# Kernel optimization log

Measured on AMD Instinct MI355X. Metric: run time of the kernel, lower is better.

The kernel has to match this reference:

```python
import jax, jax.numpy as jnp
import numpy as np

EPS = 1e-5


def gcn_conv(x, W, b, src, dst, ew, num_nodes):
    """GCNConv with add_self_loops=True, symmetric normalization (PyG default)."""
    # degree at destination, self-loop weight 1.0 included implicitly
    deg = jax.ops.segment_sum(ew, dst, num_segments=num_nodes) + 1.0  # [N]
    dinv = jax.lax.rsqrt(deg)                                         # deg >= 1
    norm = dinv[src] * ew * dinv[dst]                                 # [E]
    h = x @ W                                                         # [N, F]
    msg = norm[:, None] * h[src]                                      # [E, F]
    agg = jax.ops.segment_sum(msg, dst, num_segments=num_nodes)       # [N, F]
    # self-loop contribution: dinv[i] * 1 * dinv[i] = 1/deg[i]
    agg = agg + h * (1.0 / deg)[:, None]
    return agg + b


def batchnorm(h, gamma, beta):
    mean = jnp.mean(h, axis=0)
    var = jnp.mean(jnp.square(h - mean), axis=0)  # biased, training-mode stats
    return (h - mean) * jax.lax.rsqrt(var + EPS) * gamma + beta


def setup_inputs() -> dict:
    key = jax.random.key(0)
    ks = jax.random.split(key, 8)
    N, E, F = 50000, 800000, 64
    x = jax.random.normal(ks[0], (N, F), dtype=jnp.float32)
    edge_index = jax.random.randint(ks[1], (2, E), 0, N, dtype=jnp.int64)
    edge_weight = jax.random.uniform(ks[2], (E,), dtype=jnp.float32)
    s = 1.0 / np.sqrt(F)
    W1 = jax.random.uniform(ks[3], (F, F), jnp.float32, -s, s)
    b1 = jnp.zeros((F,), jnp.float32)
    W2 = jax.random.uniform(ks[4], (F, F), jnp.float32, -s, s)
    b2 = jnp.zeros((F,), jnp.float32)
    gamma1 = jnp.ones((F,), jnp.float32)
    beta1 = jnp.zeros((F,), jnp.float32)
    gamma2 = jnp.ones((F,), jnp.float32)
    beta2 = jnp.zeros((F,), jnp.float32)
    return {"x": x, "edge_index": edge_index, "edge_weight": edge_weight,
            "W1": W1, "b1": b1, "gamma1": gamma1, "beta1": beta1,
            "W2": W2, "b2": b2, "gamma2": gamma2, "beta2": beta2}


def reference(x, edge_index, edge_weight, W1, b1, gamma1, beta1, W2, b2, gamma2, beta2):
    N = x.shape[0]
    src, dst = edge_index[0], edge_index[1]
    identity = x
    out = gcn_conv(x, W1, b1, src, dst, edge_weight, N)
    out = jax.nn.relu(batchnorm(out, gamma1, beta1))
    out = gcn_conv(out, W2, b2, src, dst, edge_weight, N)
    out = batchnorm(out, gamma2, beta2)
    out = out + identity  # residual: num_input_features == hidden_dim
    return jax.nn.relu(out)
```

## Files before the change

kernel.cpp:

```cpp
#include <hip/hip_runtime.h>
#include <math.h>

#define FEAT 64
#define BN_EPS 1e-5f
#define BN_REPS 64
#define CNT_REPS 4

__device__ __forceinline__ int edge_idx(const void* p, int is64, long long i) {
    return is64 ? (int)((const long long*)p)[i] : ((const int*)p)[i];
}

__device__ __forceinline__ float4 f4fma(float a, float4 b, float4 c) {
    return make_float4(fmaf(a, b.x, c.x), fmaf(a, b.y, c.y),
                       fmaf(a, b.z, c.z), fmaf(a, b.w, c.w));
}

__device__ __forceinline__ unsigned bf16rtne(float f) {
    unsigned u = __float_as_uint(f);
    return (u + 0x7fffu + ((u >> 16) & 1u)) >> 16;
}
__device__ __forceinline__ unsigned packbf2(float a, float b) {
    return bf16rtne(a) | (bf16rtne(b) << 16);
}
__device__ __forceinline__ float4 unpackbf4(uint2 r) {
    return make_float4(__uint_as_float(r.x << 16),
                       __uint_as_float(r.x & 0xffff0000u),
                       __uint_as_float(r.y << 16),
                       __uint_as_float(r.y & 0xffff0000u));
}

__global__ __launch_bounds__(256) void init_kernel(
    const unsigned* __restrict__ w, int* __restrict__ flag,
    int* __restrict__ cnt, float* __restrict__ parts, int N4) {
    int i = blockIdx.x * 256 + threadIdx.x;
    if (i < N4) cnt[i] = 0;
    if (blockIdx.x < 64) parts[blockIdx.x * 256 + threadIdx.x] = 0.0f;
    if (blockIdx.x == 0 && threadIdx.x < 64) {
        unsigned long long ok = __ballot(w[2 * threadIdx.x + 1] == 0u);
        if (threadIdx.x == 0) *flag = (ok == ~0ull);
    }
}

__global__ __launch_bounds__(256) void fused_count_gemm1_kernel(
    const void* __restrict__ ei, const int* __restrict__ flag,
    int* __restrict__ cnt, int* __restrict__ seq, int E,
    const float* __restrict__ x, const float* __restrict__ W1,
    uint2* __restrict__ out_bf, int N, int nc) {
    __shared__ float4 Ws4[64][16];
    __shared__ float xs[64][65];
    int tid = threadIdx.x;

    if ((int)blockIdx.x < nc) {
        int is64 = *flag;
        int T = nc * 256;
        int i = blockIdx.x * 256 + tid;
#pragma unroll
        for (int u = 0; u < 8; ++u) {
            int e = i + u * T;
            if (e < E) {
                int dst = edge_idx(ei, is64, (long long)E + e);
                seq[e] = atomicAdd(&cnt[(e & 3) * N + dst], 1);
            }
        }
        return;
    }

    int gb = blockIdx.x - nc;
    const float4* W4 = (const float4*)W1;
    for (int j = tid; j < 1024; j += 256) Ws4[j >> 4][j & 15] = W4[j];
    __syncthreads();

    int rowBase = gb * 64;
    for (int j = tid; j < 1024; j += 256) {
        int r = j >> 4, q = j & 15;
        int row = rowBase + r;
        float4 v = make_float4(0.f, 0.f, 0.f, 0.f);
        if (row < N) v = ((const float4*)x)[(size_t)row * 16 + q];
        xs[r][q * 4 + 0] = v.x;
        xs[r][q * 4 + 1] = v.y;
        xs[r][q * 4 + 2] = v.z;
        xs[r][q * 4 + 3] = v.w;
    }
    __syncthreads();

    int q = tid & 15, rg = tid >> 4;
    int r0 = rg * 4;
    float4 a0 = make_float4(0.f, 0.f, 0.f, 0.f), a1 = a0, a2 = a0, a3 = a0;
#pragma unroll 4
    for (int k = 0; k < 64; ++k) {
        float4 wv = Ws4[k][q];
        a0 = f4fma(xs[r0 + 0][k], wv, a0);
        a1 = f4fma(xs[r0 + 1][k], wv, a1);
        a2 = f4fma(xs[r0 + 2][k], wv, a2);
        a3 = f4fma(xs[r0 + 3][k], wv, a3);
    }
    int row = rowBase + r0;
    if (row + 0 < N) out_bf[(size_t)(row + 0) * 16 + q] = make_uint2(packbf2(a0.x, a0.y), packbf2(a0.z, a0.w));
    if (row + 1 < N) out_bf[(size_t)(row + 1) * 16 + q] = make_uint2(packbf2(a1.x, a1.y), packbf2(a1.z, a1.w));
    if (row + 2 < N) out_bf[(size_t)(row + 2) * 16 + q] = make_uint2(packbf2(a2.x, a2.y), packbf2(a2.z, a2.w));
    if (row + 3 < N) out_bf[(size_t)(row + 3) * 16 + q] = make_uint2(packbf2(a3.x, a3.y), packbf2(a3.z, a3.w));
}

__global__ __launch_bounds__(256) void scan1_kernel(const int* __restrict__ cnt,
                                                    int* __restrict__ excl,
                                                    int* __restrict__ bsum,
                                                    int N, int N4) {
    __shared__ int tmp[256];
    int j = blockIdx.x * 256 + threadIdx.x;
    int v = (j < N4) ? cnt[(j & 3) * N + (j >> 2)] : 0;
    tmp[threadIdx.x] = v;
    __syncthreads();
    for (int off = 1; off < 256; off <<= 1) {
        int t = (threadIdx.x >= off) ? tmp[threadIdx.x - off] : 0;
        __syncthreads();
        tmp[threadIdx.x] += t;
        __syncthreads();
    }
    if (j < N4) excl[j] = tmp[threadIdx.x] - v;
    if (threadIdx.x == 255) bsum[blockIdx.x] = tmp[255];
}

__global__ __launch_bounds__(256) void scan3_kernel(const int* __restrict__ excl,
                                                    const int* __restrict__ bsum,
                                                    int* __restrict__ rptrR,
                                                    int N4, int E, int nb) {
    __shared__ int red[256];
    int tid = threadIdx.x;
    int s = 0;
#pragma unroll
    for (int k = tid; k < 1024; k += 256)
        if (k < nb && k < (int)blockIdx.x) s += bsum[k];
    red[tid] = s;
    __syncthreads();
    for (int off = 128; off > 0; off >>= 1) {
        if (tid < off) red[tid] += red[tid + off];
        __syncthreads();
    }
    int base = red[0];
    int j = blockIdx.x * 256 + tid;
    if (j < N4) rptrR[j] = excl[j] + base;
    if (blockIdx.x == 0 && tid == 0) rptrR[N4] = E;
}

__global__ __launch_bounds__(256) void scatter_csr_kernel(
    const void* __restrict__ ei, const float* __restrict__ ew,
    const int* __restrict__ flag, const int* __restrict__ rptrR,
    const int* __restrict__ seq, unsigned* __restrict__ csr, int E) {
    int is64 = *flag;
    int T = gridDim.x * 256;
    int i = blockIdx.x * 256 + threadIdx.x;
#pragma unroll
    for (int u = 0; u < 2; ++u) {
        int e = i + u * T;
        if (e < E) {
            int src = edge_idx(ei, is64, e);
            int dst = edge_idx(ei, is64, (long long)E + e);
            int pos = rptrR[(dst << 2) | (e & 3)] + seq[e];
            csr[pos] = (unsigned)src | (bf16rtne(ew[e]) << 16);
        }
    }
}

__global__ __launch_bounds__(256) void deg_inv_kernel(
    const int* __restrict__ rptrR, const unsigned* __restrict__ csr,
    float* __restrict__ dinv, float* __restrict__ invdeg, int N) {
    int t = blockIdx.x * 256 + threadIdx.x;
    int n = t >> 3, l = t & 7;
    if (n >= N) return;
    int b = rptrR[n << 2], e = rptrR[(n << 2) + 4];
    float d = 0.0f;
    for (int k = b + l; k < e; k += 8)
        d += __uint_as_float(csr[k] & 0xffff0000u);
    d += __shfl_xor(d, 1);
    d += __shfl_xor(d, 2);
    d += __shfl_xor(d, 4);
    if (l == 0) {
        d += 1.0f;
        dinv[n]   = rsqrtf(d);
        invdeg[n] = 1.0f / d;
    }
}

__global__ __launch_bounds__(256) void fold_kernel(unsigned* __restrict__ csr,
                                                   const float* __restrict__ dinv,
                                                   int E) {
    int T = gridDim.x * 256;
    int i = blockIdx.x * 256 + threadIdx.x;
#pragma unroll
    for (int u = 0; u < 2; ++u) {
        int e = i + u * T;
        if (e < E) {
            unsigned v = csr[e];
            float nrm = dinv[v & 0xffffu] * __uint_as_float(v & 0xffff0000u);
            csr[e] = (v & 0xffffu) | (bf16rtne(nrm) << 16);
        }
    }
}

__global__ __launch_bounds__(256) void gemm2_kernel(
    const uint2* __restrict__ in_bf, const float* __restrict__ W,
    const float* __restrict__ parts, const float* __restrict__ gamma,
    const float* __restrict__ beta, uint2* __restrict__ out_bf,
    int N, float invN) {
    __shared__ float4 Ws4[64][16];
    __shared__ float xs[64][65];
    __shared__ float sA[64], sS[64];
    int tid = threadIdx.x;
    const float4* W4 = (const float4*)W;
    for (int j = tid; j < 1024; j += 256) Ws4[j >> 4][j & 15] = W4[j];
    if (tid < 64) {
        float sm = 0.f, sq = 0.f;
#pragma unroll
        for (int r = 0; r < BN_REPS; ++r) {
            sm += parts[r * 128 + tid];
            sq += parts[r * 128 + 64 + tid];
        }
        float m = sm * invN;
        float var = fmaxf(sq * invN - m * m, 0.0f);
        float aa = gamma[tid] * rsqrtf(var + BN_EPS);
        sA[tid] = aa;
        sS[tid] = beta[tid] - m * aa;
    }
    __syncthreads();

    int rowBase = blockIdx.x * 64;
    for (int j = tid; j < 1024; j += 256) {
        int r = j >> 4, q = j & 15;
        int row = rowBase + r;
        float4 v = make_float4(0.f, 0.f, 0.f, 0.f);
        if (row < N) {
            v = unpackbf4(in_bf[(size_t)row * 16 + q]);
            int c = q * 4;
            v.x = fmaxf(fmaf(v.x, sA[c + 0], sS[c + 0]), 0.f);
            v.y = fmaxf(fmaf(v.y, sA[c + 1], sS[c + 1]), 0.f);
            v.z = fmaxf(fmaf(v.z, sA[c + 2], sS[c + 2]), 0.f);
            v.w = fmaxf(fmaf(v.w, sA[c + 3], sS[c + 3]), 0.f);
        }
        xs[r][q * 4 + 0] = v.x;
        xs[r][q * 4 + 1] = v.y;
        xs[r][q * 4 + 2] = v.z;
        xs[r][q * 4 + 3] = v.w;
    }
    __syncthreads();

    int q = tid & 15, rg = tid >> 4;
    int r0 = rg * 4;
    float4 a0 = make_float4(0.f, 0.f, 0.f, 0.f), a1 = a0, a2 = a0, a3 = a0;
#pragma unroll 4
    for (int k = 0; k < 64; ++k) {
        float4 wv = Ws4[k][q];
        a0 = f4fma(xs[r0 + 0][k], wv, a0);
        a1 = f4fma(xs[r0 + 1][k], wv, a1);
        a2 = f4fma(xs[r0 + 2][k], wv, a2);
        a3 = f4fma(xs[r0 + 3][k], wv, a3);
    }
    int row = rowBase + r0;
    if (row + 0 < N) out_bf[(size_t)(row + 0) * 16 + q] = make_uint2(packbf2(a0.x, a0.y), packbf2(a0.z, a0.w));
    if (row + 1 < N) out_bf[(size_t)(row + 1) * 16 + q] = make_uint2(packbf2(a1.x, a1.y), packbf2(a1.z, a1.w));
    if (row + 2 < N) out_bf[(size_t)(row + 2) * 16 + q] = make_uint2(packbf2(a2.x, a2.y), packbf2(a2.z, a2.w));
    if (row + 3 < N) out_bf[(size_t)(row + 3) * 16 + q] = make_uint2(packbf2(a3.x, a3.y), packbf2(a3.z, a3.w));
}

template <int OBF>
__global__ __launch_bounds__(256) void gather_agg_kernel(
    const uint2* __restrict__ h2, const int* __restrict__ rptrR,
    const unsigned* __restrict__ csr, const float* __restrict__ dinv,
    const float* __restrict__ invdeg, const float* __restrict__ bias,
    void* __restrict__ aggout, float* __restrict__ parts, int N) {
    int tid = threadIdx.x;
    int wave = tid >> 6, lane = tid & 63;
    int sub = lane >> 4, sl = lane & 15;
    float4 bv = ((const float4*)bias)[sl];
    float4 bnS = make_float4(0.f, 0.f, 0.f, 0.f), bnQ = bnS;

    int n0 = blockIdx.x * 16 + wave * 4;
#pragma unroll
    for (int i = 0; i < 4; ++i) {
        int n = n0 + i;
        if (n >= N) break;
        int beg = rptrR[n << 2], end = rptrR[(n << 2) + 4];
        uint2 selfr = h2[(size_t)n * 16 + sl];
        float dn = dinv[n], idg = invdeg[n];

        float4 accE = make_float4(0.f, 0.f, 0.f, 0.f);
        for (int k = beg; k < end; k += 32) {
            int srcs[8]; float w[8];
#pragma unroll
            for (int j = 0; j < 8; ++j) {
                int idx = k + sub + 4 * j;
                if (idx < end) {
                    unsigned v = __builtin_nontemporal_load(&csr[idx]);
                    srcs[j] = (int)(v & 0xffffu);
                    w[j] = __uint_as_float(v & 0xffff0000u);
                } else { srcs[j] = 0; w[j] = 0.f; }
            }
            uint2 hr[8];
#pragma unroll
            for (int j = 0; j < 8; ++j)
                hr[j] = (k + sub + 4 * j < end)
                          ? h2[(size_t)srcs[j] * 16 + sl] : make_uint2(0u, 0u);
#pragma unroll
            for (int j = 0; j < 8; ++j)
                accE = f4fma(w[j], unpackbf4(hr[j]), accE);
        }
        accE.x += __shfl_xor(accE.x, 16); accE.y += __shfl_xor(accE.y, 16);
        accE.z += __shfl_xor(accE.z, 16); accE.w += __shfl_xor(accE.w, 16);
        accE.x += __shfl_xor(accE.x, 32); accE.y += __shfl_xor(accE.y, 32);
        accE.z += __shfl_xor(accE.z, 32); accE.w += __shfl_xor(accE.w, 32);

        if (sub == 0) {
            float4 self = unpackbf4(selfr);
            float4 tot = f4fma(idg, self, bv);
            tot = f4fma(dn, accE, tot);
            if (OBF) {
                ((uint2*)aggout)[(size_t)n * 16 + sl] =
                    make_uint2(packbf2(tot.x, tot.y), packbf2(tot.z, tot.w));
            } else {
                ((float4*)aggout)[(size_t)n * 16 + sl] = tot;
            }
            bnS.x += tot.x; bnS.y += tot.y; bnS.z += tot.z; bnS.w += tot.w;
            bnQ.x = fmaf(tot.x, tot.x, bnQ.x); bnQ.y = fmaf(tot.y, tot.y, bnQ.y);
            bnQ.z = fmaf(tot.z, tot.z, bnQ.z); bnQ.w = fmaf(tot.w, tot.w, bnQ.w);
        }
    }

    __shared__ float4 LS[4][16], LQ[4][16];
    if (sub == 0) { LS[wave][sl] = bnS; LQ[wave][sl] = bnQ; }
    __syncthreads();
    if (tid < 16) {
        float4 ts = LS[0][tid], tq = LQ[0][tid];
        for (int i = 1; i < 4; ++i) {
            float4 a = LS[i][tid], b = LQ[i][tid];
            ts.x += a.x; ts.y += a.y; ts.z += a.z; ts.w += a.w;
            tq.x += b.x; tq.y += b.y; tq.z += b.z; tq.w += b.w;
        }
        float* P = parts + (size_t)(blockIdx.x & (BN_REPS - 1)) * 128;
        int c = tid * 4;
        unsafeAtomicAdd(&P[c + 0], ts.x);      unsafeAtomicAdd(&P[c + 1], ts.y);
        unsafeAtomicAdd(&P[c + 2], ts.z);      unsafeAtomicAdd(&P[c + 3], ts.w);
        unsafeAtomicAdd(&P[64 + c + 0], tq.x); unsafeAtomicAdd(&P[64 + c + 1], tq.y);
        unsafeAtomicAdd(&P[64 + c + 2], tq.z); unsafeAtomicAdd(&P[64 + c + 3], tq.w);
    }
}

__global__ __launch_bounds__(256) void final_out_kernel(
    const float* __restrict__ agg, const float* __restrict__ parts,
    const float* __restrict__ gamma, const float* __restrict__ beta,
    const float* __restrict__ x, float* __restrict__ out,
    int nquads, float invN) {
    __shared__ float sA[64], sS[64];
    int tid = threadIdx.x;
    if (tid < 64) {
        float sm = 0.f, sq = 0.f;
#pragma unroll
        for (int r = 0; r < BN_REPS; ++r) {
            sm += parts[r * 128 + tid];
            sq += parts[r * 128 + 64 + tid];
        }
        float m = sm * invN;
        float var = fmaxf(sq * invN - m * m, 0.0f);
        float aa = gamma[tid] * rsqrtf(var + BN_EPS);
        sA[tid] = aa;
        sS[tid] = beta[tid] - m * aa;
    }
    __syncthreads();
    int gid = blockIdx.x * 256 + tid;
    if (gid < nquads) {
        int c = (gid & 15) * 4;
        float4 g = ((const float4*)agg)[gid], xv = ((const float4*)x)[gid];
        float4 o;
        o.x = fmaxf(fmaf(g.x, sA[c + 0], sS[c + 0]) + xv.x, 0.f);
        o.y = fmaxf(fmaf(g.y, sA[c + 1], sS[c + 1]) + xv.y, 0.f);
        o.z = fmaxf(fmaf(g.z, sA[c + 2], sS[c + 2]) + xv.z, 0.f);
        o.w = fmaxf(fmaf(g.w, sA[c + 3], sS[c + 3]) + xv.w, 0.f);
        ((float4*)out)[gid] = o;
    }
}

extern "C" void kernel_launch(void* const* d_in, const int* in_sizes, int n_in,
                              void* d_out, int out_size, void* d_ws, size_t ws_size,
                              hipStream_t stream) {
    const float* x      = (const float*)d_in[0];
    const void*  ei     = d_in[1];
    const float* ew     = (const float*)d_in[2];
    const float* W1     = (const float*)d_in[3];
    const float* b1     = (const float*)d_in[4];
    const float* gamma1 = (const float*)d_in[5];
    const float* beta1  = (const float*)d_in[6];
    const float* W2     = (const float*)d_in[7];
    const float* b2     = (const float*)d_in[8];
    const float* gamma2 = (const float*)d_in[9];
    const float* beta2  = (const float*)d_in[10];
    float* out = (float*)d_out;

    const int N = in_sizes[0] / FEAT;
    const int E = in_sizes[2];
    const int N4 = N * CNT_REPS;

    char* ws = (char*)d_ws;
    size_t off = 0;
    auto alloc = [&](size_t bytes) {
        size_t o = off;
        off += (bytes + 255) & ~(size_t)255;
        return (void*)(ws + o);
    };
    int*      flag   = (int*)     alloc(256);
    int*      cnt    = (int*)     alloc((size_t)N4 * 4);
    int*      rptrR  = (int*)     alloc((size_t)(N4 + 1) * 4);
    int*      seq    = (int*)     alloc((size_t)E * 4);
    int*      excl   = (int*)     alloc((size_t)N4 * 4);
    int*      bsum   = (int*)     alloc(1024 * 4);
    float*    dinv   = (float*)   alloc((size_t)N * 4);
    float*    invdeg = (float*)   alloc((size_t)N * 4);
    float*    parts  = (float*)   alloc(2 * BN_REPS * 128 * 4);
    unsigned* csr    = (unsigned*)alloc((size_t)E * 4);
    uint2*    h_bf   = (uint2*)   alloc((size_t)N * 16 * 8);
    uint2*    agg_bf = (uint2*)   alloc((size_t)N * 16 * 8);
    float*    agg    = (float*)   alloc((size_t)N * FEAT * 4);

    const int nblkN4 = (N4 + 255) / 256;
    const int nblkE2 = (E + 511) / 512;
    const int nblkQ  = (N * 16 + 255) / 256;
    const int nblkG  = (N + 63) / 64;
    const int nblkA  = (N + 15) / 16;
    const int nc     = (E + 2047) / 2048;
    const float invN = 1.0f / (float)N;

    init_kernel<<<nblkN4, 256, 0, stream>>>((const unsigned*)ei, flag, cnt, parts, N4);
    fused_count_gemm1_kernel<<<nc + nblkG, 256, 0, stream>>>(
        ei, flag, cnt, seq, E, x, W1, h_bf, N, nc);
    scan1_kernel<<<nblkN4, 256, 0, stream>>>(cnt, excl, bsum, N, N4);
    scan3_kernel<<<nblkN4, 256, 0, stream>>>(excl, bsum, rptrR, N4, E, nblkN4);
    scatter_csr_kernel<<<nblkE2, 256, 0, stream>>>(ei, ew, flag, rptrR, seq, csr, E);
    deg_inv_kernel<<<(N * 8 + 255) / 256, 256, 0, stream>>>(rptrR, csr, dinv, invdeg, N);
    fold_kernel<<<nblkE2, 256, 0, stream>>>(csr, dinv, E);

    gather_agg_kernel<1><<<nblkA, 256, 0, stream>>>(h_bf, rptrR, csr, dinv,
                                                    invdeg, b1, agg_bf, parts, N);
    gemm2_kernel<<<nblkG, 256, 0, stream>>>(agg_bf, W2, parts, gamma1, beta1,
                                            h_bf, N, invN);
    gather_agg_kernel<0><<<nblkA, 256, 0, stream>>>(h_bf, rptrR, csr, dinv,
                                                    invdeg, b2, agg,
                                                    parts + BN_REPS * 128, N);
    final_out_kernel<<<nblkQ, 256, 0, stream>>>(agg, parts + BN_REPS * 128,
                                                gamma2, beta2, x, out,
                                                N * 16, invN);
}
```

Before: 181.1 us.

## Fold source-side dinv into node features instead of per-edge CSR weights

Drops the per-edge fold kernel that multiplied each CSR weight by dinv[src]. Instead, the degree kernel now prescales the first-layer bf16 features by dinv per node, and gemm2 scales its output rows by dinv. The gather then computes dinv[n]*(sum w*h' + h'_self), which removes the separate invdeg array. This trades a pass over the E edges for a pass over N rows and one fewer kernel launch, at the cost of an extra bf16 rounding of the scaled features.

Result: faster. 176.7 us (-2.4%).

```diff
diff --git a/kernel.cpp b/kernel.cpp
--- a/kernel.cpp
+++ b/kernel.cpp
@@ -161,38 +161,38 @@
     }
 }
 
-__global__ __launch_bounds__(256) void deg_inv_kernel(
+__global__ __launch_bounds__(256) void deg_inv_scale_kernel(
     const int* __restrict__ rptrR, const unsigned* __restrict__ csr,
-    float* __restrict__ dinv, float* __restrict__ invdeg, int N) {
-    int t = blockIdx.x * 256 + threadIdx.x;
-    int n = t >> 3, l = t & 7;
-    if (n >= N) return;
-    int b = rptrR[n << 2], e = rptrR[(n << 2) + 4];
-    float d = 0.0f;
-    for (int k = b + l; k < e; k += 8)
-        d += __uint_as_float(csr[k] & 0xffff0000u);
-    d += __shfl_xor(d, 1);
-    d += __shfl_xor(d, 2);
-    d += __shfl_xor(d, 4);
-    if (l == 0) {
-        d += 1.0f;
-        dinv[n]   = rsqrtf(d);
-        invdeg[n] = 1.0f / d;
-    }
-}
-
-__global__ __launch_bounds__(256) void fold_kernel(unsigned* __restrict__ csr,
-                                                   const float* __restrict__ dinv,
-                                                   int E) {
-    int T = gridDim.x * 256;
-    int i = blockIdx.x * 256 + threadIdx.x;
-#pragma unroll
-    for (int u = 0; u < 2; ++u) {
-        int e = i + u * T;
-        if (e < E) {
-            unsigned v = csr[e];
-            float nrm = dinv[v & 0xffffu] * __uint_as_float(v & 0xffff0000u);
-            csr[e] = (v & 0xffffu) | (bf16rtne(nrm) << 16);
+    float* __restrict__ dinv, uint2* __restrict__ h_bf, int N) {
+    __shared__ float sd[32];
+    int tid = threadIdx.x;
+    int n = blockIdx.x * 32 + (tid >> 3), l = tid & 7;
+    if (n < N) {
+        int b = rptrR[n << 2], e = rptrR[(n << 2) + 4];
+        float d = 0.0f;
+        for (int k = b + l; k < e; k += 8)
+            d += __uint_as_float(csr[k] & 0xffff0000u);
+        d += __shfl_xor(d, 1);
+        d += __shfl_xor(d, 2);
+        d += __shfl_xor(d, 4);
+        if (l == 0) {
+            float dv = rsqrtf(1.0f + d);
+            dinv[n] = dv;
+            sd[tid >> 3] = dv;
+        }
+    }
+    __syncthreads();
+    int rg = tid >> 4, sl = tid & 15;
+#pragma unroll
+    for (int p = 0; p < 2; ++p) {
+        int m = p * 16 + rg;
+        int row = blockIdx.x * 32 + m;
+        if (row < N) {
+            float dv = sd[m];
+            size_t idx = (size_t)row * 16 + sl;
+            float4 v = unpackbf4(h_bf[idx]);
+            h_bf[idx] = make_uint2(packbf2(dv * v.x, dv * v.y),
+                                   packbf2(dv * v.z, dv * v.w));
         }
     }
 }
@@ -200,8 +200,8 @@
 __global__ __launch_bounds__(256) void gemm2_kernel(
     const uint2* __restrict__ in_bf, const float* __restrict__ W,
     const float* __restrict__ parts, const float* __restrict__ gamma,
-    const float* __restrict__ beta, uint2* __restrict__ out_bf,
-    int N, float invN) {
+    const float* __restrict__ beta, const float* __restrict__ dinv,
+    uint2* __restrict__ out_bf, int N, float invN) {
     __shared__ float4 Ws4[64][16];
     __shared__ float xs[64][65];
     __shared__ float sA[64], sS[64];
@@ -255,17 +255,17 @@
         a3 = f4fma(xs[r0 + 3][k], wv, a3);
     }
     int row = rowBase + r0;
-    if (row + 0 < N) out_bf[(size_t)(row + 0) * 16 + q] = make_uint2(packbf2(a0.x, a0.y), packbf2(a0.z, a0.w));
-    if (row + 1 < N) out_bf[(size_t)(row + 1) * 16 + q] = make_uint2(packbf2(a1.x, a1.y), packbf2(a1.z, a1.w));
-    if (row + 2 < N) out_bf[(size_t)(row + 2) * 16 + q] = make_uint2(packbf2(a2.x, a2.y), packbf2(a2.z, a2.w));
-    if (row + 3 < N) out_bf[(size_t)(row + 3) * 16 + q] = make_uint2(packbf2(a3.x, a3.y), packbf2(a3.z, a3.w));
+    if (row + 0 < N) { float d = dinv[row + 0]; out_bf[(size_t)(row + 0) * 16 + q] = make_uint2(packbf2(d * a0.x, d * a0.y), packbf2(d * a0.z, d * a0.w)); }
+    if (row + 1 < N) { float d = dinv[row + 1]; out_bf[(size_t)(row + 1) * 16 + q] = make_uint2(packbf2(d * a1.x, d * a1.y), packbf2(d * a1.z, d * a1.w)); }
+    if (row + 2 < N) { float d = dinv[row + 2]; out_bf[(size_t)(row + 2) * 16 + q] = make_uint2(packbf2(d * a2.x, d * a2.y), packbf2(d * a2.z, d * a2.w)); }
+    if (row + 3 < N) { float d = dinv[row + 3]; out_bf[(size_t)(row + 3) * 16 + q] = make_uint2(packbf2(d * a3.x, d * a3.y), packbf2(d * a3.z, d * a3.w)); }
 }
 
 template <int OBF>
 __global__ __launch_bounds__(256) void gather_agg_kernel(
     const uint2* __restrict__ h2, const int* __restrict__ rptrR,
     const unsigned* __restrict__ csr, const float* __restrict__ dinv,
-    const float* __restrict__ invdeg, const float* __restrict__ bias,
+    const float* __restrict__ bias,
     void* __restrict__ aggout, float* __restrict__ parts, int N) {
     int tid = threadIdx.x;
     int wave = tid >> 6, lane = tid & 63;
@@ -280,7 +280,7 @@
         if (n >= N) break;
         int beg = rptrR[n << 2], end = rptrR[(n << 2) + 4];
         uint2 selfr = h2[(size_t)n * 16 + sl];
-        float dn = dinv[n], idg = invdeg[n];
+        float dn = dinv[n];
 
         float4 accE = make_float4(0.f, 0.f, 0.f, 0.f);
         for (int k = beg; k < end; k += 32) {
@@ -310,8 +310,11 @@
 
         if (sub == 0) {
             float4 self = unpackbf4(selfr);
-            float4 tot = f4fma(idg, self, bv);
-            tot = f4fma(dn, accE, tot);
+            float4 tot;
+            tot.x = fmaf(dn, accE.x + self.x, bv.x);
+            tot.y = fmaf(dn, accE.y + self.y, bv.y);
+            tot.z = fmaf(dn, accE.z + self.z, bv.z);
+            tot.w = fmaf(dn, accE.w + self.w, bv.w);
             if (OBF) {
                 ((uint2*)aggout)[(size_t)n * 16 + sl] =
                     make_uint2(packbf2(tot.x, tot.y), packbf2(tot.z, tot.w));
@@ -411,7 +414,6 @@
     int*      excl   = (int*)     alloc((size_t)N4 * 4);
     int*      bsum   = (int*)     alloc(1024 * 4);
     float*    dinv   = (float*)   alloc((size_t)N * 4);
-    float*    invdeg = (float*)   alloc((size_t)N * 4);
     float*    parts  = (float*)   alloc(2 * BN_REPS * 128 * 4);
     unsigned* csr    = (unsigned*)alloc((size_t)E * 4);
     uint2*    h_bf   = (uint2*)   alloc((size_t)N * 16 * 8);
@@ -423,6 +425,7 @@
     const int nblkQ  = (N * 16 + 255) / 256;
     const int nblkG  = (N + 63) / 64;
     const int nblkA  = (N + 15) / 16;
+    const int nblkD  = (N + 31) / 32;
     const int nc     = (E + 2047) / 2048;
     const float invN = 1.0f / (float)N;
 
@@ -432,15 +435,14 @@
     scan1_kernel<<<nblkN4, 256, 0, stream>>>(cnt, excl, bsum, N, N4);
     scan3_kernel<<<nblkN4, 256, 0, stream>>>(excl, bsum, rptrR, N4, E, nblkN4);
     scatter_csr_kernel<<<nblkE2, 256, 0, stream>>>(ei, ew, flag, rptrR, seq, csr, E);
-    deg_inv_kernel<<<(N * 8 + 255) / 256, 256, 0, stream>>>(rptrR, csr, dinv, invdeg, N);
-    fold_kernel<<<nblkE2, 256, 0, stream>>>(csr, dinv, E);
+    deg_inv_scale_kernel<<<nblkD, 256, 0, stream>>>(rptrR, csr, dinv, h_bf, N);
 
     gather_agg_kernel<1><<<nblkA, 256, 0, stream>>>(h_bf, rptrR, csr, dinv,
-                                                    invdeg, b1, agg_bf, parts, N);
+                                                    b1, agg_bf, parts, N);
     gemm2_kernel<<<nblkG, 256, 0, stream>>>(agg_bf, W2, parts, gamma1, beta1,
-                                            h_bf, N, invN);
+                                            dinv, h_bf, N, invN);
     gather_agg_kernel<0><<<nblkA, 256, 0, stream>>>(h_bf, rptrR, csr, dinv,
-                                                    invdeg, b2, agg,
+                                                    b2, agg,
                                                     parts + BN_REPS * 128, N);
     final_out_kernel<<<nblkQ, 256, 0, stream>>>(agg, parts + BN_REPS * 128,
                                                 gamma2, beta2, x, out,
```
